# Performance work log

Measured on AMD Instinct MI355X. Metric: run time of the kernel, lower is better.

The kernel has to match this reference:

```python
import jax, jax.numpy as jnp
import numpy as np

B, S, H, I, E, K = 1, 2048, 1024, 2048, 8, 2


def setup_inputs() -> dict:
    key = jax.random.key(0)
    k0, k1, k2, k3, k4 = jax.random.split(key, 5)
    x = jax.random.normal(k0, (B, S, H), dtype=jnp.float32)
    Wg = jax.random.normal(k1, (H, E), dtype=jnp.float32) * 0.02   # gate (no bias)
    W1 = jax.random.normal(k2, (E, H, I), dtype=jnp.float32) * 0.02  # expert up
    W3 = jax.random.normal(k3, (E, H, I), dtype=jnp.float32) * 0.02  # expert gate
    W2 = jax.random.normal(k4, (E, I, H), dtype=jnp.float32) * 0.02  # expert down
    return {"x": x, "Wg": Wg, "W1": W1, "W2": W2, "W3": W3}


def reference(x, Wg, W1, W2, W3):
    b, s, h = x.shape
    e = Wg.shape[1]
    xf = x.reshape(-1, h)                      # (T, H)
    T = xf.shape[0]

    # Router: top-2 logits, softmax over the 2 selected logits (fp32), cast back.
    logits = xf @ Wg                           # (T, E)
    top_vals, top_idx = jax.lax.top_k(logits, K)
    rw = jax.nn.softmax(top_vals.astype(jnp.float32), axis=-1).astype(x.dtype)  # (T, K)

    # Dense per-expert combine weight: w[t, e] = routing weight if expert e selected, else 0.
    w = jnp.zeros((T, e), dtype=x.dtype).at[jnp.arange(T)[:, None], top_idx].add(rw)

    # Expert MLPs computed for all experts, zero-weighted tokens contribute nothing
    # (mathematically identical to the gather/MLP/scatter-add in the torch loop).
    up = jnp.einsum('th,ehi->tei', xf, W1)     # (T, E, I)
    gate = jnp.einsum('th,ehi->tei', xf, W3)   # (T, E, I)
    act = jax.nn.silu(up) * gate               # (T, E, I)
    out = jnp.einsum('tei,eih,te->th', act, W2, w)  # (T, H)
    return out.reshape(b, s, h)
```

## Files before the change

kernel.cpp:

```cpp
#include <hip/hip_runtime.h>
#include <math.h>

#define NUM_TOK 2048
#define HDIM 1024
#define IDIM 2048
#define NEXP 8
#define MAX_ROWS 5120
#define NTM 40

typedef __attribute__((ext_vector_type(8))) short bf16x8;
typedef __attribute__((ext_vector_type(4))) float f32x4;

#define OFF_IDX   0u
#define OFF_RW    16384u
#define OFF_SEG   32832u
#define OFF_ROWS  33024u
#define OFF_POS   53504u
#define OFF_XB    131072u
#define OFF_ACT   109051904u
#define OFF_SO    8388608u

__device__ __forceinline__ unsigned short f2bf(float f) {
  __bf16 b = (__bf16)f;
  return __builtin_bit_cast(unsigned short, b);
}

__device__ __forceinline__ unsigned pk2(float lo, float hi) {
  __bf16 a = (__bf16)lo, b = (__bf16)hi;
  return (unsigned)__builtin_bit_cast(unsigned short, a) |
         ((unsigned)__builtin_bit_cast(unsigned short, b) << 16);
}

__device__ __forceinline__ void gld16(const void* g, void* l) {
  __builtin_amdgcn_global_load_lds(
      (const __attribute__((address_space(1))) void*)g,
      (__attribute__((address_space(3))) void*)l, 16, 0, 0);
}


__global__ void k_router(const float* __restrict__ x, const float* __restrict__ wg,
                         unsigned short* __restrict__ xb,
                         int* __restrict__ idx, float* __restrict__ rw) {
  const int wave = threadIdx.x >> 6, lane = threadIdx.x & 63;
  const int t = blockIdx.x * 4 + wave;
  const float2* __restrict__ xr = (const float2*)(x + (size_t)t * HDIM);
  unsigned* __restrict__ xbr = (unsigned*)(xb + (size_t)t * HDIM);
  float acc[8];
#pragma unroll
  for (int q = 0; q < 8; ++q) acc[q] = 0.f;
#pragma unroll
  for (int j = 0; j < 8; ++j) {
    const int h2 = lane + (j << 6);
    const float2 v = xr[h2];
    const float* wrow = wg + (size_t)h2 * 16;
    const float4 a0 = *(const float4*)(wrow);
    const float4 a1 = *(const float4*)(wrow + 4);
    const float4 b0 = *(const float4*)(wrow + 8);
    const float4 b1 = *(const float4*)(wrow + 12);
    acc[0] = fmaf(v.x, a0.x, fmaf(v.y, b0.x, acc[0]));
    acc[1] = fmaf(v.x, a0.y, fmaf(v.y, b0.y, acc[1]));
    acc[2] = fmaf(v.x, a0.z, fmaf(v.y, b0.z, acc[2]));
    acc[3] = fmaf(v.x, a0.w, fmaf(v.y, b0.w, acc[3]));
    acc[4] = fmaf(v.x, a1.x, fmaf(v.y, b1.x, acc[4]));
    acc[5] = fmaf(v.x, a1.y, fmaf(v.y, b1.y, acc[5]));
    acc[6] = fmaf(v.x, a1.z, fmaf(v.y, b1.z, acc[6]));
    acc[7] = fmaf(v.x, a1.w, fmaf(v.y, b1.w, acc[7]));
    xbr[h2] = pk2(v.x, v.y);
  }
#pragma unroll
  for (int q = 0; q < 8; ++q) {
#pragma unroll
    for (int off = 32; off >= 1; off >>= 1)
      acc[q] += __shfl_xor(acc[q], off, 64);
  }
  if (lane == 0) {
    int i0 = 0; float v0 = acc[0];
#pragma unroll
    for (int q = 1; q < 8; ++q)
      if (acc[q] > v0) { v0 = acc[q]; i0 = q; }
    int i1 = -1; float v1 = -3.4e38f;
#pragma unroll
    for (int q = 0; q < 8; ++q)
      if (q != i0 && acc[q] > v1) { v1 = acc[q]; i1 = q; }
    const float e1 = expf(v1 - v0);
    const float inv = 1.f / (1.f + e1);
    idx[2 * t] = i0; idx[2 * t + 1] = i1;
    rw[2 * t] = inv; rw[2 * t + 1] = e1 * inv;
  }
}

__global__ void k_segscatter(const int* __restrict__ idx, int* __restrict__ seg,
                             int* __restrict__ rowsv, int* __restrict__ pos) {
  __shared__ int hist[NEXP], cur[NEXP], sseg[NEXP];
  const int tid = threadIdx.x;
  if (tid < NEXP) { hist[tid] = 0; cur[tid] = 0; }
  __syncthreads();
  for (int s = tid; s < 2 * NUM_TOK; s += 256) atomicAdd(&hist[idx[s]], 1);
  for (int r = tid; r < MAX_ROWS; r += 256) rowsv[r] = -1;
  __syncthreads();
  if (tid == 0) {
    int s = 0;
    for (int q = 0; q < NEXP; ++q) {
      seg[q] = s; sseg[q] = s;
      s += ((hist[q] + 127) / 128) * 128;
    }
    seg[NEXP] = s;
  }
  __syncthreads();
  for (int s = tid; s < 2 * NUM_TOK; s += 256) {
    const int e = idx[s];
    const int p = atomicAdd(&cur[e], 1);
    const int rr = sseg[e] + p;
    rowsv[rr] = s;
    pos[s] = rr;
  }
}

__launch_bounds__(256, 2)
__global__ void k_gemm1(const unsigned short* __restrict__ xb,
                        const float* __restrict__ W1f,
                        const float* __restrict__ W3f,
                        const int* __restrict__ seg, const int* __restrict__ rowsv,
                        unsigned short* __restrict__ act) {
  __shared__ __align__(16) unsigned short As[2][128 * 32];
  __shared__ __align__(16) unsigned short Bs[2][128 * 32];
  const int tid = threadIdx.x;
  const int w = tid >> 6, l = tid & 63;
  const int m0 = blockIdx.y * 128;
  const int total = seg[NEXP];
  if (m0 >= total) return;
  int e = 0;
#pragma unroll
  for (int q = 1; q < NEXP; ++q) if (m0 >= seg[q]) e = q;
  const int n0 = blockIdx.x * 64;

  const int swzA = ((l & 3) ^ ((l >> 4) & 3) ^ ((l >> 3) & 3)) * 8;
  size_t aOff[2];
#pragma unroll
  for (int q = 0; q < 2; ++q) {
    const int r = rowsv[m0 + w * 32 + q * 16 + (l >> 2)];
    const int tk = (r < 0) ? 0 : (r >> 1);
    aOff[q] = (size_t)tk * HDIM + swzA;
  }
  const int kk = tid >> 4;
  const int ng = tid & 15;
  const size_t bBase = (size_t)e * HDIM * IDIM + (size_t)(2 * kk) * IDIM + n0 + ng * 4;

  struct Bregs { float4 u0, u1, g0, g1; };
  auto loadB = [&](Bregs& p, int k0) {
    const size_t b = bBase + (size_t)k0 * IDIM;
    p.u0 = *(const float4*)(W1f + b);
    p.u1 = *(const float4*)(W1f + b + IDIM);
    p.g0 = *(const float4*)(W3f + b);
    p.g1 = *(const float4*)(W3f + b + IDIM);
  };
  auto writeB = [&](int buf, const Bregs& p) {
    unsigned* Bd = (unsigned*)&Bs[buf][0];
    const float a0[4] = {p.u0.x, p.u0.y, p.u0.z, p.u0.w};
    const float a1[4] = {p.u1.x, p.u1.y, p.u1.z, p.u1.w};
    const float c0[4] = {p.g0.x, p.g0.y, p.g0.z, p.g0.w};
    const float c1[4] = {p.g1.x, p.g1.y, p.g1.z, p.g1.w};
#pragma unroll
    for (int i = 0; i < 4; ++i) {
      const int r = ng * 4 + i;
      const int f = ((r >> 2) & 3) ^ ((r >> 1) & 3);
      const int d = (((kk >> 2) ^ f) << 2) + (kk & 3);
      Bd[r * 16 + d]        = pk2(a0[i], a1[i]);
      Bd[(r + 64) * 16 + d] = pk2(c0[i], c1[i]);
    }
  };
  auto stageA = [&](int buf, int k0) {
#pragma unroll
    for (int q = 0; q < 2; ++q)
      gld16(xb + aOff[q] + k0, &As[buf][(w * 32 + q * 16) * 32]);
  };

  f32x4 acc[2][8];
#pragma unroll
  for (int m = 0; m < 2; ++m)
#pragma unroll
    for (int nf = 0; nf < 8; ++nf) acc[m][nf] = (f32x4)0.f;

  const int rslot = ((l >> 4) ^ ((l >> 2) & 3) ^ ((l >> 1) & 3)) * 8;
  const int arow = (w * 32 + (l & 15)) * 32 + rslot;
  auto mfmaStep = [&](int buf) {
    const bf16x8 a0 = *(const bf16x8*)&As[buf][arow];
    const bf16x8 a1 = *(const bf16x8*)&As[buf][arow + 16 * 32];
#pragma unroll
    for (int nf = 0; nf < 8; ++nf) {
      const bf16x8 b = *(const bf16x8*)&Bs[buf][(nf * 16 + (l & 15)) * 32 + rslot];
      acc[0][nf] = __builtin_amdgcn_mfma_f32_16x16x32_bf16(a0, b, acc[0][nf], 0, 0, 0);
      acc[1][nf] = __builtin_amdgcn_mfma_f32_16x16x32_bf16(a1, b, acc[1][nf], 0, 0, 0);
    }
  };

  Bregs pA, pB;
  loadB(pA, 0);
  stageA(0, 0);
  loadB(pB, 32);
  writeB(0, pA);
  __syncthreads();

  const int NT = HDIM / 32;
  for (int t = 0; t < NT; t += 2) {
    if (t + 2 < NT) loadB(pA, (t + 2) * 32);
    stageA(1, (t + 1) * 32);
    __builtin_amdgcn_sched_barrier(0);
    mfmaStep(0);
    writeB(1, pB);
    __syncthreads();
    if (t + 3 < NT) loadB(pB, (t + 3) * 32);
    if (t + 2 < NT) stageA(0, (t + 2) * 32);
    __builtin_amdgcn_sched_barrier(0);
    mfmaStep(1);
    if (t + 2 < NT) writeB(0, pA);
    __syncthreads();
  }
  const int rbase = m0 + w * 32 + (l >> 4) * 4;
  const int cbase = n0 + (l & 15);
#pragma unroll
  for (int m = 0; m < 2; ++m)
#pragma unroll
    for (int p = 0; p < 4; ++p) {
      const f32x4 up = acc[m][p];
      const f32x4 gt = acc[m][p + 4];
#pragma unroll
      for (int r = 0; r < 4; ++r) {
        const float u = up[r];
        const float s = (u / (1.f + expf(-u))) * gt[r];
        act[(size_t)(rbase + m * 16 + r) * IDIM + cbase + p * 16] = f2bf(s);
      }
    }
}

__launch_bounds__(256, 2)
__global__ void k_gemm2(const unsigned short* __restrict__ act,
                        const float* __restrict__ W2f,
                        const int* __restrict__ seg,
                        float* __restrict__ so) {
  __shared__ __align__(16) unsigned short As[2][128 * 32];
  __shared__ __align__(16) unsigned short Bs[2][128 * 32];
  const int tid = threadIdx.x;
  const int w = tid >> 6, l = tid & 63;
  const int m0 = blockIdx.y * 128;
  const int total = seg[NEXP];
  if (m0 >= total) return;
  int e = 0;
#pragma unroll
  for (int q = 1; q < NEXP; ++q) if (m0 >= seg[q]) e = q;
  const int n0 = blockIdx.x * 128;

  const int swzA = ((tid & 3) ^ ((tid >> 4) & 3) ^ ((tid >> 3) & 3)) * 8;
  size_t aOff[2];
#pragma unroll
  for (int q = 0; q < 2; ++q)
    aOff[q] = (size_t)(m0 + q * 64 + (tid >> 2)) * IDIM + swzA;

  const int kk = tid >> 4;
  const int ng = tid & 15;
  const size_t bBase = (size_t)e * IDIM * HDIM + (size_t)(2 * kk) * HDIM + n0 + ng * 4;

  struct Bregs { float4 a0, a1, b0, b1; };
  auto loadB = [&](Bregs& p, int k0) {
    const size_t b = bBase + (size_t)k0 * HDIM;
    p.a0 = *(const float4*)(W2f + b);
    p.a1 = *(const float4*)(W2f + b + HDIM);
    p.b0 = *(const float4*)(W2f + b + 64);
    p.b1 = *(const float4*)(W2f + b + HDIM + 64);
  };
  auto writeB = [&](int buf, const Bregs& p) {
    unsigned* Bd = (unsigned*)&Bs[buf][0];
    const float q00[4] = {p.a0.x, p.a0.y, p.a0.z, p.a0.w};
    const float q01[4] = {p.a1.x, p.a1.y, p.a1.z, p.a1.w};
    const float q10[4] = {p.b0.x, p.b0.y, p.b0.z, p.b0.w};
    const float q11[4] = {p.b1.x, p.b1.y, p.b1.z, p.b1.w};
#pragma unroll
    for (int i = 0; i < 4; ++i) {
      const int rm = ng * 4 + i;
      const int f = ((rm >> 2) & 3) ^ ((rm >> 1) & 3);
      const int d = (((kk >> 2) ^ f) << 2) + (kk & 3);
      Bd[rm * 16 + d]        = pk2(q00[i], q01[i]);
      Bd[(rm + 64) * 16 + d] = pk2(q10[i], q11[i]);
    }
  };
  auto stageA = [&](int buf, int k0) {
#pragma unroll
    for (int q = 0; q < 2; ++q)
      gld16(act + aOff[q] + k0, &As[buf][(q * 64 + (tid >> 2)) * 32]);
  };

  f32x4 acc[2][8];
#pragma unroll
  for (int mf = 0; mf < 2; ++mf)
#pragma unroll
    for (int nf = 0; nf < 8; ++nf) acc[mf][nf] = (f32x4)0.f;

  const int rslot = ((l >> 4) ^ ((l >> 2) & 3) ^ ((l >> 1) & 3)) * 8;
  const int arow = (w * 32 + (l & 15)) * 32 + rslot;
  auto mfmaStep = [&](int buf) {
    const bf16x8 a0 = *(const bf16x8*)&As[buf][arow];
    const bf16x8 a1 = *(const bf16x8*)&As[buf][arow + 16 * 32];
#pragma unroll
    for (int nf = 0; nf < 8; ++nf) {
      const bf16x8 b = *(const bf16x8*)&Bs[buf][(nf * 16 + (l & 15)) * 32 + rslot];
      acc[0][nf] = __builtin_amdgcn_mfma_f32_16x16x32_bf16(a0, b, acc[0][nf], 0, 0, 0);
      acc[1][nf] = __builtin_amdgcn_mfma_f32_16x16x32_bf16(a1, b, acc[1][nf], 0, 0, 0);
    }
  };

  Bregs pA, pB;
  loadB(pA, 0);
  stageA(0, 0);
  loadB(pB, 32);
  writeB(0, pA);
  __syncthreads();

  const int NT = IDIM / 32;
  for (int t = 0; t < NT; t += 2) {
    if (t + 2 < NT) loadB(pA, (t + 2) * 32);
    stageA(1, (t + 1) * 32);
    __builtin_amdgcn_sched_barrier(0);
    mfmaStep(0);
    writeB(1, pB);
    __syncthreads();
    if (t + 3 < NT) loadB(pB, (t + 3) * 32);
    if (t + 2 < NT) stageA(0, (t + 2) * 32);
    __builtin_amdgcn_sched_barrier(0);
    mfmaStep(1);
    if (t + 2 < NT) writeB(0, pA);
    __syncthreads();
  }
  const int rbase = m0 + w * 32 + (l >> 4) * 4;
  const int cbase = n0 + (l & 15);
#pragma unroll
  for (int mf = 0; mf < 2; ++mf)
#pragma unroll
    for (int nf = 0; nf < 8; ++nf)
#pragma unroll
      for (int r = 0; r < 4; ++r)
        so[(size_t)(rbase + mf * 16 + r) * HDIM + cbase + nf * 16] = acc[mf][nf][r];
}

__global__ void k_combine(const float* __restrict__ so, const int* __restrict__ pos,
                          const float* __restrict__ rw, float* __restrict__ out) {
  const int t = blockIdx.x, i = threadIdx.x;
  const int p0 = pos[2 * t], p1 = pos[2 * t + 1];
  const float w0 = rw[2 * t], w1 = rw[2 * t + 1];
  const float4 a = ((const float4*)(so + (size_t)p0 * HDIM))[i];
  const float4 b = ((const float4*)(so + (size_t)p1 * HDIM))[i];
  float4 o;
  o.x = w0 * a.x + w1 * b.x;
  o.y = w0 * a.y + w1 * b.y;
  o.z = w0 * a.z + w1 * b.z;
  o.w = w0 * a.w + w1 * b.w;
  ((float4*)(out + (size_t)t * HDIM))[i] = o;
}

extern "C" void kernel_launch(void* const* d_in, const int* in_sizes, int n_in,
                              void* d_out, int out_size, void* d_ws, size_t ws_size,
                              hipStream_t stream) {
  const float* x  = (const float*)d_in[0];
  const float* Wg = (const float*)d_in[1];
  const float* W1 = (const float*)d_in[2];
  const float* W2 = (const float*)d_in[3];
  const float* W3 = (const float*)d_in[4];
  float* out = (float*)d_out;
  char* ws = (char*)d_ws;
  int*   idx  = (int*)(ws + OFF_IDX);
  float* rw   = (float*)(ws + OFF_RW);
  int*   seg  = (int*)(ws + OFF_SEG);
  int*   rowsv= (int*)(ws + OFF_ROWS);
  int*   pos  = (int*)(ws + OFF_POS);
  unsigned short* xb  = (unsigned short*)(ws + OFF_XB);
  unsigned short* act = (unsigned short*)(ws + OFF_ACT);
  float* so = (float*)(ws + OFF_SO);

  k_router<<<NUM_TOK / 4, 256, 0, stream>>>(x, Wg, xb, idx, rw);
  k_segscatter<<<1, 256, 0, stream>>>(idx, seg, rowsv, pos);
  k_gemm1<<<dim3(IDIM / 64, NTM), 256, 0, stream>>>(xb, W1, W3, seg, rowsv, act);
  k_gemm2<<<dim3(HDIM / 128, NTM), 256, 0, stream>>>(act, W2, seg, so);
  k_combine<<<NUM_TOK, 256, 0, stream>>>(so, pos, rw, out);
}
```

Measured before the change: 161.3 us.

## Double the K tile in gemm1 to 64 with a new LDS swizzle and single-stage prefetch

The up/gate GEMM now stages 64-wide K slices of A and B per iteration instead of 32, with a new 3-bit XOR swizzle for both LDS tiles. The two-register-set B prefetch is replaced by a single prefetch one tile ahead. This halves the number of barrier-separated iterations and gives more MFMA work per sync. In exchange LDS use doubles to 64KB per block, which may limit occupancy, and the shallower register prefetch may expose more global load latency.

```diff
diff --git a/kernel.cpp b/kernel.cpp
--- a/kernel.cpp
+++ b/kernel.cpp
@@ -36,7 +36,6 @@
       (const __attribute__((address_space(1))) void*)g,
       (__attribute__((address_space(3))) void*)l, 16, 0, 0);
 }
-
 
 __global__ void k_router(const float* __restrict__ x, const float* __restrict__ wg,
                          unsigned short* __restrict__ xb,
@@ -122,8 +121,8 @@
                         const float* __restrict__ W3f,
                         const int* __restrict__ seg, const int* __restrict__ rowsv,
                         unsigned short* __restrict__ act) {
-  __shared__ __align__(16) unsigned short As[2][128 * 32];
-  __shared__ __align__(16) unsigned short Bs[2][128 * 32];
+  __shared__ __align__(16) unsigned short As[2][128 * 64];
+  __shared__ __align__(16) unsigned short Bs[2][128 * 64];
   const int tid = threadIdx.x;
   const int w = tid >> 6, l = tid & 63;
   const int m0 = blockIdx.y * 128;
@@ -134,45 +133,50 @@
   for (int q = 1; q < NEXP; ++q) if (m0 >= seg[q]) e = q;
   const int n0 = blockIdx.x * 64;
 
-  const int swzA = ((l & 3) ^ ((l >> 4) & 3) ^ ((l >> 3) & 3)) * 8;
-  size_t aOff[2];
-#pragma unroll
-  for (int q = 0; q < 2; ++q) {
-    const int r = rowsv[m0 + w * 32 + q * 16 + (l >> 2)];
-    const int tk = (r < 0) ? 0 : (r >> 1);
-    aOff[q] = (size_t)tk * HDIM + swzA;
-  }
-  const int kk = tid >> 4;
-  const int ng = tid & 15;
-  const size_t bBase = (size_t)e * HDIM * IDIM + (size_t)(2 * kk) * IDIM + n0 + ng * 4;
-
-  struct Bregs { float4 u0, u1, g0, g1; };
-  auto loadB = [&](Bregs& p, int k0) {
+  size_t aOff[4];
+#pragma unroll
+  for (int q = 0; q < 4; ++q) {
+    const int r = 32 * q + (tid >> 3);
+    const int rv = rowsv[m0 + r];
+    const int tk = (rv < 0) ? 0 : (rv >> 1);
+    const int sc = (tid & 7) ^ (r & 7) ^ ((r >> 3) & 7);
+    aOff[q] = (size_t)tk * HDIM + sc * 8;
+  }
+  auto stageA = [&](int buf, int k0) {
+#pragma unroll
+    for (int q = 0; q < 4; ++q)
+      gld16(xb + aOff[q] + k0, &As[buf][(32 * q + 8 * w) * 64 + l * 8]);
+  };
+
+  const int kk = tid >> 3;
+  const int ng = tid & 7;
+  const size_t bBase = (size_t)e * HDIM * IDIM + (size_t)(2 * kk) * IDIM + n0 + ng * 8;
+  float4 u0a, u0b, u1a, u1b, g0a, g0b, g1a, g1b;
+  auto loadB = [&](int k0) {
     const size_t b = bBase + (size_t)k0 * IDIM;
-    p.u0 = *(const float4*)(W1f + b);
-    p.u1 = *(const float4*)(W1f + b + IDIM);
-    p.g0 = *(const float4*)(W3f + b);
-    p.g1 = *(const float4*)(W3f + b + IDIM);
-  };
-  auto writeB = [&](int buf, const Bregs& p) {
+    u0a = *(const float4*)(W1f + b);
+    u0b = *(const float4*)(W1f + b + 4);
+    u1a = *(const float4*)(W1f + b + IDIM);
+    u1b = *(const float4*)(W1f + b + IDIM + 4);
+    g0a = *(const float4*)(W3f + b);
+    g0b = *(const float4*)(W3f + b + 4);
+    g1a = *(const float4*)(W3f + b + IDIM);
+    g1b = *(const float4*)(W3f + b + IDIM + 4);
+  };
+  auto writeB = [&](int buf) {
     unsigned* Bd = (unsigned*)&Bs[buf][0];
-    const float a0[4] = {p.u0.x, p.u0.y, p.u0.z, p.u0.w};
-    const float a1[4] = {p.u1.x, p.u1.y, p.u1.z, p.u1.w};
-    const float c0[4] = {p.g0.x, p.g0.y, p.g0.z, p.g0.w};
-    const float c1[4] = {p.g1.x, p.g1.y, p.g1.z, p.g1.w};
-#pragma unroll
-    for (int i = 0; i < 4; ++i) {
-      const int r = ng * 4 + i;
-      const int f = ((r >> 2) & 3) ^ ((r >> 1) & 3);
-      const int d = (((kk >> 2) ^ f) << 2) + (kk & 3);
-      Bd[r * 16 + d]        = pk2(a0[i], a1[i]);
-      Bd[(r + 64) * 16 + d] = pk2(c0[i], c1[i]);
-    }
-  };
-  auto stageA = [&](int buf, int k0) {
-#pragma unroll
-    for (int q = 0; q < 2; ++q)
-      gld16(xb + aOff[q] + k0, &As[buf][(w * 32 + q * 16) * 32]);
+    const float a0[8] = {u0a.x, u0a.y, u0a.z, u0a.w, u0b.x, u0b.y, u0b.z, u0b.w};
+    const float a1[8] = {u1a.x, u1a.y, u1a.z, u1a.w, u1b.x, u1b.y, u1b.z, u1b.w};
+    const float c0[8] = {g0a.x, g0a.y, g0a.z, g0a.w, g0b.x, g0b.y, g0b.z, g0b.w};
+    const float c1[8] = {g1a.x, g1a.y, g1a.z, g1a.w, g1b.x, g1b.y, g1b.z, g1b.w};
+#pragma unroll
+    for (int j = 0; j < 8; ++j) {
+      const int r = ng * 8 + j;
+      const int pc = (kk >> 2) ^ (r & 7) ^ ((r >> 3) & 7);
+      const int d = pc * 4 + (kk & 3);
+      Bd[r * 32 + d]          = pk2(a0[j], a1[j]);
+      Bd[(r + 64) * 32 + d]   = pk2(c0[j], c1[j]);
+    }
   };
 
   f32x4 acc[2][8];
@@ -181,41 +185,47 @@
 #pragma unroll
     for (int nf = 0; nf < 8; ++nf) acc[m][nf] = (f32x4)0.f;
 
-  const int rslot = ((l >> 4) ^ ((l >> 2) & 3) ^ ((l >> 1) & 3)) * 8;
-  const int arow = (w * 32 + (l & 15)) * 32 + rslot;
   auto mfmaStep = [&](int buf) {
-    const bf16x8 a0 = *(const bf16x8*)&As[buf][arow];
-    const bf16x8 a1 = *(const bf16x8*)&As[buf][arow + 16 * 32];
-#pragma unroll
-    for (int nf = 0; nf < 8; ++nf) {
-      const bf16x8 b = *(const bf16x8*)&Bs[buf][(nf * 16 + (l & 15)) * 32 + rslot];
-      acc[0][nf] = __builtin_amdgcn_mfma_f32_16x16x32_bf16(a0, b, acc[0][nf], 0, 0, 0);
-      acc[1][nf] = __builtin_amdgcn_mfma_f32_16x16x32_bf16(a1, b, acc[1][nf], 0, 0, 0);
-    }
-  };
-
-  Bregs pA, pB;
-  loadB(pA, 0);
+#pragma unroll
+    for (int kh = 0; kh < 2; ++kh) {
+      const int c = kh * 4 + (l >> 4);
+      bf16x8 a[2], b[8];
+#pragma unroll
+      for (int m = 0; m < 2; ++m) {
+        const int Ra = 32 * w + 16 * m + (l & 15);
+        const int pA = c ^ (Ra & 7) ^ ((Ra >> 3) & 7);
+        a[m] = *(const bf16x8*)&As[buf][Ra * 64 + pA * 8];
+      }
+#pragma unroll
+      for (int nf = 0; nf < 8; ++nf) {
+        const int Rb = nf * 16 + (l & 15);
+        const int pB = c ^ (Rb & 7) ^ ((Rb >> 3) & 7);
+        b[nf] = *(const bf16x8*)&Bs[buf][Rb * 64 + pB * 8];
+      }
+#pragma unroll
+      for (int m = 0; m < 2; ++m)
+#pragma unroll
+        for (int nf = 0; nf < 8; ++nf)
+          acc[m][nf] = __builtin_amdgcn_mfma_f32_16x16x32_bf16(a[m], b[nf], acc[m][nf], 0, 0, 0);
+    }
+  };
+
   stageA(0, 0);
-  loadB(pB, 32);
-  writeB(0, pA);
-  __syncthreads();
-
-  const int NT = HDIM / 32;
-  for (int t = 0; t < NT; t += 2) {
-    if (t + 2 < NT) loadB(pA, (t + 2) * 32);
-    stageA(1, (t + 1) * 32);
+  loadB(0);
+  writeB(0);
+  __syncthreads();
+
+  const int NT = HDIM / 64;
+  for (int t = 0; t < NT; ++t) {
+    const int cur = t & 1;
+    if (t + 1 < NT) { stageA(cur ^ 1, (t + 1) * 64); loadB((t + 1) * 64); }
     __builtin_amdgcn_sched_barrier(0);
-    mfmaStep(0);
-    writeB(1, pB);
+    mfmaStep(cur);
+    __builtin_amdgcn_sched_barrier(0);
+    if (t + 1 < NT) writeB(cur ^ 1);
     __syncthreads();
-    if (t + 3 < NT) loadB(pB, (t + 3) * 32);
-    if (t + 2 < NT) stageA(0, (t + 2) * 32);
-    __builtin_amdgcn_sched_barrier(0);
-    mfmaStep(1);
-    if (t + 2 < NT) writeB(0, pA);
-    __syncthreads();
-  }
+  }
+
   const int rbase = m0 + w * 32 + (l >> 4) * 4;
   const int cbase = n0 + (l & 15);
 #pragma unroll
```

New measurement: 163.9 us. Within noise of the previous version (+1.6%).

## Enlarge gemm1 M tile to 256 rows with 512-thread blocks and split W1/W3 loads

Applied to the files above, without the earlier changes.

The gate/up GEMM now uses 256-row M tiles and 8 waves per block, with half the threads loading W1 and half loading W3 into shared memory. Each block converts and stages a B tile once and reuses it across twice as many token rows, cutting redundant fp32 weight reads and bf16 conversion. Expert segments are padded to 256 rows, so MAX_ROWS grows and workspace offsets shift. The cost is more padded rows per expert, doubled A shared memory, and tighter register limits under launch_bounds(512,4).

```diff
diff --git a/kernel.cpp b/kernel.cpp
--- a/kernel.cpp
+++ b/kernel.cpp
@@ -5,8 +5,7 @@
 #define HDIM 1024
 #define IDIM 2048
 #define NEXP 8
-#define MAX_ROWS 5120
-#define NTM 40
+#define MAX_ROWS 6144
 
 typedef __attribute__((ext_vector_type(8))) short bf16x8;
 typedef __attribute__((ext_vector_type(4))) float f32x4;
@@ -15,10 +14,10 @@
 #define OFF_RW    16384u
 #define OFF_SEG   32832u
 #define OFF_ROWS  33024u
-#define OFF_POS   53504u
+#define OFF_POS   57600u
 #define OFF_XB    131072u
-#define OFF_ACT   109051904u
 #define OFF_SO    8388608u
+#define OFF_ACT   41943040u
 
 __device__ __forceinline__ unsigned short f2bf(float f) {
   __bf16 b = (__bf16)f;
@@ -36,7 +35,6 @@
       (const __attribute__((address_space(1))) void*)g,
       (__attribute__((address_space(3))) void*)l, 16, 0, 0);
 }
-
 
 __global__ void k_router(const float* __restrict__ x, const float* __restrict__ wg,
                          unsigned short* __restrict__ xb,
@@ -102,7 +100,7 @@
     int s = 0;
     for (int q = 0; q < NEXP; ++q) {
       seg[q] = s; sseg[q] = s;
-      s += ((hist[q] + 127) / 128) * 128;
+      s += ((hist[q] + 255) / 256) * 256;
     }
     seg[NEXP] = s;
   }
@@ -116,17 +114,17 @@
   }
 }
 
-__launch_bounds__(256, 2)
+__launch_bounds__(512, 4)
 __global__ void k_gemm1(const unsigned short* __restrict__ xb,
                         const float* __restrict__ W1f,
                         const float* __restrict__ W3f,
                         const int* __restrict__ seg, const int* __restrict__ rowsv,
                         unsigned short* __restrict__ act) {
-  __shared__ __align__(16) unsigned short As[2][128 * 32];
+  __shared__ __align__(16) unsigned short As[2][256 * 32];
   __shared__ __align__(16) unsigned short Bs[2][128 * 32];
   const int tid = threadIdx.x;
   const int w = tid >> 6, l = tid & 63;
-  const int m0 = blockIdx.y * 128;
+  const int m0 = blockIdx.y * 256;
   const int total = seg[NEXP];
   if (m0 >= total) return;
   int e = 0;
@@ -134,45 +132,43 @@
   for (int q = 1; q < NEXP; ++q) if (m0 >= seg[q]) e = q;
   const int n0 = blockIdx.x * 64;
 
-  const int swzA = ((l & 3) ^ ((l >> 4) & 3) ^ ((l >> 3) & 3)) * 8;
+  const int swzA = ((tid & 3) ^ ((tid >> 4) & 3) ^ ((tid >> 3) & 3)) * 8;
   size_t aOff[2];
 #pragma unroll
   for (int q = 0; q < 2; ++q) {
-    const int r = rowsv[m0 + w * 32 + q * 16 + (l >> 2)];
+    const int r = rowsv[m0 + q * 128 + (tid >> 2)];
     const int tk = (r < 0) ? 0 : (r >> 1);
     aOff[q] = (size_t)tk * HDIM + swzA;
   }
-  const int kk = tid >> 4;
+  auto stageA = [&](int buf, int k0) {
+#pragma unroll
+    for (int q = 0; q < 2; ++q)
+      gld16(xb + aOff[q] + k0, &As[buf][(q * 128 + (tid >> 2)) * 32 + (tid & 3) * 8]);
+  };
+
+  const int s  = tid >> 8;
+  const int kk = (tid >> 4) & 15;
   const int ng = tid & 15;
+  const float* __restrict__ Wf = s ? W3f : W1f;
   const size_t bBase = (size_t)e * HDIM * IDIM + (size_t)(2 * kk) * IDIM + n0 + ng * 4;
 
-  struct Bregs { float4 u0, u1, g0, g1; };
+  struct Bregs { float4 v0, v1; };
   auto loadB = [&](Bregs& p, int k0) {
     const size_t b = bBase + (size_t)k0 * IDIM;
-    p.u0 = *(const float4*)(W1f + b);
-    p.u1 = *(const float4*)(W1f + b + IDIM);
-    p.g0 = *(const float4*)(W3f + b);
-    p.g1 = *(const float4*)(W3f + b + IDIM);
+    p.v0 = *(const float4*)(Wf + b);
+    p.v1 = *(const float4*)(Wf + b + IDIM);
   };
   auto writeB = [&](int buf, const Bregs& p) {
     unsigned* Bd = (unsigned*)&Bs[buf][0];
-    const float a0[4] = {p.u0.x, p.u0.y, p.u0.z, p.u0.w};
-    const float a1[4] = {p.u1.x, p.u1.y, p.u1.z, p.u1.w};
-    const float c0[4] = {p.g0.x, p.g0.y, p.g0.z, p.g0.w};
-    const float c1[4] = {p.g1.x, p.g1.y, p.g1.z, p.g1.w};
+    const float a0[4] = {p.v0.x, p.v0.y, p.v0.z, p.v0.w};
+    const float a1[4] = {p.v1.x, p.v1.y, p.v1.z, p.v1.w};
 #pragma unroll
     for (int i = 0; i < 4; ++i) {
-      const int r = ng * 4 + i;
+      const int r = s * 64 + ng * 4 + i;
       const int f = ((r >> 2) & 3) ^ ((r >> 1) & 3);
       const int d = (((kk >> 2) ^ f) << 2) + (kk & 3);
-      Bd[r * 16 + d]        = pk2(a0[i], a1[i]);
-      Bd[(r + 64) * 16 + d] = pk2(c0[i], c1[i]);
-    }
-  };
-  auto stageA = [&](int buf, int k0) {
-#pragma unroll
-    for (int q = 0; q < 2; ++q)
-      gld16(xb + aOff[q] + k0, &As[buf][(w * 32 + q * 16) * 32]);
+      Bd[r * 16 + d] = pk2(a0[i], a1[i]);
+    }
   };
 
   f32x4 acc[2][8];
@@ -216,6 +212,7 @@
     if (t + 2 < NT) writeB(0, pA);
     __syncthreads();
   }
+
   const int rbase = m0 + w * 32 + (l >> 4) * 4;
   const int cbase = n0 + (l & 15);
 #pragma unroll
@@ -227,8 +224,8 @@
 #pragma unroll
       for (int r = 0; r < 4; ++r) {
         const float u = up[r];
-        const float s = (u / (1.f + expf(-u))) * gt[r];
-        act[(size_t)(rbase + m * 16 + r) * IDIM + cbase + p * 16] = f2bf(s);
+        const float sv = (u / (1.f + expf(-u))) * gt[r];
+        act[(size_t)(rbase + m * 16 + r) * IDIM + cbase + p * 16] = f2bf(sv);
       }
     }
 }
@@ -377,7 +374,7 @@
 
   k_router<<<NUM_TOK / 4, 256, 0, stream>>>(x, Wg, xb, idx, rw);
   k_segscatter<<<1, 256, 0, stream>>>(idx, seg, rowsv, pos);
-  k_gemm1<<<dim3(IDIM / 64, NTM), 256, 0, stream>>>(xb, W1, W3, seg, rowsv, act);
-  k_gemm2<<<dim3(HDIM / 128, NTM), 256, 0, stream>>>(act, W2, seg, so);
+  k_gemm1<<<dim3(IDIM / 64, MAX_ROWS / 256), 512, 0, stream>>>(xb, W1, W3, seg, rowsv, act);
+  k_gemm2<<<dim3(HDIM / 128, MAX_ROWS / 128), 256, 0, stream>>>(act, W2, seg, so);
   k_combine<<<NUM_TOK, 256, 0, stream>>>(so, pos, rw, out);
 }
```

Measured after the change: 161.6 us. About the same (+0.2%).
